# Kernel tuning notes

Measured on AMD Instinct MI355X. Metric: run time of the kernel, lower is better.

Reference implementation:

```python
import jax, jax.numpy as jnp
import numpy as np

N_NODES = 50000
D_IN = 128
HIDDEN = 128
UNITS_DENSE = 256
N_EDGES = 600000
N_PRED = 200000
N_SEL = 300000


def setup_inputs() -> dict:
    key = jax.random.key(0)
    ks = jax.random.split(key, 12)
    node_state = jax.random.normal(ks[0], (N_NODES, D_IN), jnp.float32)
    edge_index = jax.random.randint(ks[1], (2, N_EDGES), 0, N_NODES, jnp.int32)
    out_edges = jax.random.randint(ks[2], (2, N_PRED), 0, N_NODES, jnp.int32)
    set_idx = jnp.sort(jax.random.randint(ks[3], (N_SEL,), 0, 2 * N_PRED, jnp.int32))
    # Glorot-ish scaled weights
    W1 = jax.random.normal(ks[4], (D_IN, HIDDEN), jnp.float32) / np.float32(np.sqrt(D_IN))
    b1 = jnp.zeros((HIDDEN,), jnp.float32)
    W2 = jax.random.normal(ks[5], (HIDDEN, HIDDEN), jnp.float32) / np.float32(np.sqrt(HIDDEN))
    b2 = jnp.zeros((HIDDEN,), jnp.float32)
    dense_W = jax.random.normal(ks[6], (2 * 0 + HIDDEN, UNITS_DENSE), jnp.float32) / np.float32(np.sqrt(HIDDEN))
    dense_b = jnp.zeros((UNITS_DENSE,), jnp.float32)
    out_W = jax.random.normal(ks[7], (UNITS_DENSE, 2), jnp.float32) / np.float32(np.sqrt(UNITS_DENSE))
    out_b = jnp.zeros((2,), jnp.float32)
    return {
        "node_state": node_state, "edge_index": edge_index, "out_edges": out_edges,
        "set_idx": set_idx, "W1": W1, "b1": b1, "W2": W2, "b2": b2,
        "dense_W": dense_W, "dense_b": dense_b, "out_W": out_W, "out_b": out_b,
    }


def _graph_conv(h, src, dst, W, b):
    """DGL GraphConv, norm='both', no activation: D_in^{-1/2} A D_out^{-1/2} H W + b."""
    n = h.shape[0]
    ones = jnp.ones(src.shape[0], h.dtype)
    deg_out = jnp.clip(jax.ops.segment_sum(ones, src, num_segments=n), 1.0)  # [N]
    deg_in = jnp.clip(jax.ops.segment_sum(ones, dst, num_segments=n), 1.0)   # [N]
    h = (h * jax.lax.rsqrt(deg_out)[:, None]) @ W                            # [N, H]
    agg = jax.ops.segment_sum(h[src], dst, num_segments=n)                   # [N, H]
    return agg * jax.lax.rsqrt(deg_in)[:, None] + b


def reference(node_state, edge_index, out_edges, set_idx,
              W1, b1, W2, b2, dense_W, dense_b, out_W, out_b):
    src, dst = edge_index[0], edge_index[1]
    h = _graph_conv(node_state, src, dst, W1, b1)
    h = _graph_conv(h, src, dst, W2, b2)
    # concat along axis=0 as in the original: [2*E_pred, H]
    edge_state = jnp.concatenate([h[out_edges[0]], h[out_edges[1]]], axis=0)
    # boolean_mask replaced by equivalent gather of selected (True) rows
    edge_state_set = edge_state[set_idx]                                      # [N_SEL, H]
    hidden = jax.nn.relu(edge_state_set @ dense_W + dense_b)
    return jax.nn.softmax(hidden @ out_W + out_b, axis=-1)
```

## Files before the change

### kernel.cpp

```cpp
#include <hip/hip_runtime.h>

#define NN 50000
#define DD 128
#define NE 600000
#define NP 200000
#define NS 300000
#define NU 256
#define NBH 128
#define EPB 4688
#define NW 12500

typedef __attribute__((ext_vector_type(8))) short short8;
typedef __attribute__((ext_vector_type(4))) float floatx4;

__device__ inline float bf2f(unsigned int u16) {
    unsigned int x = u16 << 16;
    float f; __builtin_memcpy(&f, &x, 4); return f;
}
__device__ inline unsigned short f2bf(float f) {
    unsigned int x; __builtin_memcpy(&x, &f, 4);
    unsigned int lsb = (x >> 16) & 1u;
    x += 0x7fffu + lsb;
    return (unsigned short)(x >> 16);
}

__global__ __launch_bounds__(256) void k_hist(const int* __restrict__ ei,
                                              unsigned int* __restrict__ P) {
    __shared__ unsigned int hw[NW];
    int b = blockIdx.x, half = blockIdx.y, tid = threadIdx.x;
    for (int w = tid; w < NW; w += 256) hw[w] = 0;
    __syncthreads();
    const int* src = ei + (size_t)half * NE;
    int e0 = b * EPB, e1 = min(e0 + EPB, NE);
    for (int e = e0 + tid; e < e1; e += 256) {
        int s = src[e];
        atomicAdd(&hw[s >> 2], 1u << ((s & 3) * 8));
    }
    __syncthreads();
    unsigned int* Pb = P + ((size_t)half * NBH + b) * NW;
    for (int w = tid; w < NW; w += 256) Pb[w] = hw[w];
}

__global__ void k_reduce(const unsigned int* __restrict__ P, int* __restrict__ deg_in,
                         float* __restrict__ r) {
    int w = blockIdx.x * 256 + threadIdx.x;
    if (w >= 2 * NW) return;
    int half = (w >= NW);
    int wl = w - half * NW;
    const unsigned int* Ph = P + (size_t)half * NBH * NW + wl;
    int c0 = 0, c1 = 0, c2 = 0, c3 = 0;
    for (int b = 0; b < NBH; ++b) {
        unsigned int v = Ph[(size_t)b * NW];
        c0 += v & 0xff; c1 += (v >> 8) & 0xff; c2 += (v >> 16) & 0xff; c3 += v >> 24;
    }
    int nb = wl * 4;
    if (half) {
        int4 d = {c0, c1, c2, c3};
        *(int4*)(deg_in + nb) = d;
    }
    float4 rr = {rsqrtf((float)max(c0, 1)), rsqrtf((float)max(c1, 1)),
                 rsqrtf((float)max(c2, 1)), rsqrtf((float)max(c3, 1))};
    *(float4*)(r + (size_t)half * NN + nb) = rr;
}

__global__ __launch_bounds__(1024) void k_scan(const int* __restrict__ deg_in,
                                               int* __restrict__ row_ptr) {
    __shared__ int wsum[16];
    __shared__ int woff[16];
    __shared__ int carry_s;
    __shared__ int total_s;
    int tid = threadIdx.x, lane = tid & 63, w = tid >> 6;
    if (tid == 0) carry_s = 0;
    __syncthreads();
    for (int wb = 0; wb < NW; wb += 1024) {
        int i4 = wb + tid;
        int4 v = {0, 0, 0, 0};
        if (i4 < NW) v = *(const int4*)(deg_in + i4 * 4);
        int t0 = v.x, t1 = t0 + v.y, t2 = t1 + v.z, tot = t2 + v.w;
        int x = tot;
#pragma unroll
        for (int off = 1; off < 64; off <<= 1) {
            int y = __shfl_up(x, off);
            if (lane >= off) x += y;
        }
        if (lane == 63) wsum[w] = x;
        __syncthreads();
        if (w == 0 && lane < 16) {
            int s = wsum[lane];
            int xs = s;
#pragma unroll
            for (int off = 1; off < 16; off <<= 1) {
                int y = __shfl_up(xs, off);
                if (lane >= off) xs += y;
            }
            woff[lane] = xs - s;
            if (lane == 15) total_s = xs;
        }
        __syncthreads();
        if (i4 < NW) {
            int base = carry_s + woff[w] + x - tot;
            int4 o = {base, base + t0, base + t1, base + t2};
            *(int4*)(row_ptr + i4 * 4) = o;
        }
        __syncthreads();
        if (tid == 0) carry_s += total_s;
        __syncthreads();
    }
    if (tid == 0) row_ptr[NN] = carry_s;
}

__global__ void k_colscan(const unsigned int* __restrict__ Pin, const int* __restrict__ row_ptr,
                          int* __restrict__ basetab) {
    int n = blockIdx.x * 256 + threadIdx.x;
    if (n >= NN) return;
    int wl = n >> 2, sh = (n & 3) * 8;
    int run = row_ptr[n];
    for (int b = 0; b < NBH; ++b) {
        basetab[(size_t)b * NN + n] = run;
        run += (Pin[(size_t)b * NW + wl] >> sh) & 0xff;
    }
}

__global__ __launch_bounds__(256) void k_bucket2(const int* __restrict__ ei,
                                                 const int* __restrict__ basetab,
                                                 int* __restrict__ col) {
    __shared__ unsigned int cw[NW];
    int b = blockIdx.x, tid = threadIdx.x;
    for (int w = tid; w < NW; w += 256) cw[w] = 0;
    __syncthreads();
    const int* bt = basetab + (size_t)b * NN;
    int e0 = b * EPB, e1 = min(e0 + EPB, NE);
    for (int e = e0 + tid; e < e1; e += 256) {
        int s = ei[e], d = ei[NE + e];
        int sh = (d & 3) * 8;
        unsigned int old = atomicAdd(&cw[d >> 2], 1u << sh);
        int local = (old >> sh) & 0xff;
        col[bt[d] + local] = s;
    }
}

__global__ void k_castT(const float* __restrict__ src, unsigned short* __restrict__ dst,
                        int R, int C) {
    int t = blockIdx.x * 256 + threadIdx.x;
    if (t < R * C) {
        int r = t / C, c = t - r * C;
        dst[c * R + r] = f2bf(src[t]);
    }
}

template <bool ABF>
__global__ __launch_bounds__(256) void k_gemm_bf(const void* __restrict__ Ap,
                                                 const float* __restrict__ rs,
                                                 const unsigned short* __restrict__ BT,
                                                 unsigned short* __restrict__ Cm) {
    __shared__ unsigned short As[64][136];
    __shared__ unsigned short Bs[128][136];
    int tid = threadIdx.x, lane = tid & 63, wave = tid >> 6;
    int quad = lane >> 4, l16 = lane & 15;
    int row0 = blockIdx.x * 64;

    if (ABF) {
        const unsigned short* A = (const unsigned short*)Ap;
#pragma unroll
        for (int p = 0; p < 4; ++p) {
            int fid = tid + p * 256;
            int r = fid >> 4, c = fid & 15;
            int gr = row0 + r; if (gr > NN - 1) gr = NN - 1;
            *(uint4*)&As[r][c * 8] = *(const uint4*)(A + (size_t)gr * DD + c * 8);
        }
    } else {
        const float* A = (const float*)Ap;
#pragma unroll
        for (int p = 0; p < 8; ++p) {
            int fid = tid + p * 256;
            int r = fid >> 5, c = fid & 31;
            int gr = row0 + r; if (gr > NN - 1) gr = NN - 1;
            float4 v = *(const float4*)(A + (size_t)gr * DD + c * 4);
            ushort4 u;
            u.x = f2bf(v.x); u.y = f2bf(v.y); u.z = f2bf(v.z); u.w = f2bf(v.w);
            *(ushort4*)&As[r][c * 4] = u;
        }
    }
#pragma unroll
    for (int p = 0; p < 8; ++p) {
        int fid = tid + p * 256;
        int r = fid >> 4, c = fid & 15;
        *(uint4*)&Bs[r][c * 8] = *(const uint4*)(BT + (size_t)r * DD + c * 8);
    }
    __syncthreads();

    short8 af[4];
#pragma unroll
    for (int ks = 0; ks < 4; ++ks)
        af[ks] = *(const short8*)&As[wave * 16 + l16][ks * 32 + quad * 8];
    floatx4 acc[8];
#pragma unroll
    for (int nt = 0; nt < 8; ++nt) acc[nt] = (floatx4){0.f, 0.f, 0.f, 0.f};
#pragma unroll
    for (int ks = 0; ks < 4; ++ks) {
#pragma unroll
        for (int nt = 0; nt < 8; ++nt) {
            short8 bf = *(const short8*)&Bs[nt * 16 + l16][ks * 32 + quad * 8];
            acc[nt] = __builtin_amdgcn_mfma_f32_16x16x32_bf16(af[ks], bf, acc[nt], 0, 0, 0);
        }
    }
    int rbase = row0 + wave * 16 + quad * 4;
#pragma unroll
    for (int r = 0; r < 4; ++r) {
        int gr = rbase + r;
        if (gr < NN) {
            float s = rs[gr];
#pragma unroll
            for (int nt = 0; nt < 8; ++nt)
                Cm[(size_t)gr * DD + nt * 16 + l16] = f2bf(acc[nt][r] * s);
        }
    }
}

__global__ __launch_bounds__(256) void k_aggregate(const unsigned short* __restrict__ T,
                                                   const int* __restrict__ row_ptr,
                                                   const int* __restrict__ col,
                                                   const float* __restrict__ r_in,
                                                   const float* __restrict__ b,
                                                   unsigned short* __restrict__ H) {
    int node = blockIdx.x * 4 + (threadIdx.x >> 6);
    if (node >= NN) return;
    int lane = threadIdx.x & 63;
    int beg = row_ptr[node], end = row_ptr[node + 1];
    float a0 = 0.f, a1 = 0.f;
    for (int base = beg; base < end; base += 64) {
        int m = end - base; if (m > 64) m = 64;
        int myidx = (lane < m) ? col[base + lane] : 0;
        int j = 0;
        for (; j + 4 <= m; j += 4) {
            int s0 = __shfl(myidx, j), s1 = __shfl(myidx, j + 1);
            int s2 = __shfl(myidx, j + 2), s3 = __shfl(myidx, j + 3);
            unsigned int v0 = *(const unsigned int*)(T + (size_t)s0 * DD + lane * 2);
            unsigned int v1 = *(const unsigned int*)(T + (size_t)s1 * DD + lane * 2);
            unsigned int v2 = *(const unsigned int*)(T + (size_t)s2 * DD + lane * 2);
            unsigned int v3 = *(const unsigned int*)(T + (size_t)s3 * DD + lane * 2);
            a0 += bf2f(v0 & 0xffff) + bf2f(v1 & 0xffff) + bf2f(v2 & 0xffff) + bf2f(v3 & 0xffff);
            a1 += bf2f(v0 >> 16) + bf2f(v1 >> 16) + bf2f(v2 >> 16) + bf2f(v3 >> 16);
        }
        for (; j < m; ++j) {
            int s = __shfl(myidx, j);
            unsigned int v = *(const unsigned int*)(T + (size_t)s * DD + lane * 2);
            a0 += bf2f(v & 0xffff);
            a1 += bf2f(v >> 16);
        }
    }
    float rv = r_in[node];
    float o0 = a0 * rv + b[lane * 2];
    float o1 = a1 * rv + b[lane * 2 + 1];
    unsigned int packed = (unsigned int)f2bf(o0) | ((unsigned int)f2bf(o1) << 16);
    *(unsigned int*)(H + (size_t)node * DD + lane * 2) = packed;
}

__global__ __launch_bounds__(256) void k_mlp_mfma(const unsigned short* __restrict__ H2,
                                                  const unsigned short* __restrict__ BTd,
                                                  const float* __restrict__ db,
                                                  const float* __restrict__ oW,
                                                  const float* __restrict__ ob,
                                                  float* __restrict__ P) {
    __shared__ unsigned short As[64][136];
    __shared__ unsigned short Bs[128][136];
    int tid = threadIdx.x, lane = tid & 63, wave = tid >> 6;
    int quad = lane >> 4, l16 = lane & 15;
    int row0 = blockIdx.x * 64;
#pragma unroll
    for (int p = 0; p < 4; ++p) {
        int fid = tid + p * 256;
        int r = fid >> 4, c = fid & 15;
        int gr = row0 + r; if (gr > NN - 1) gr = NN - 1;
        *(uint4*)&As[r][c * 8] = *(const uint4*)(H2 + (size_t)gr * DD + c * 8);
    }
    short8 af[4];
    floatx4 acc[16];
#pragma unroll
    for (int i = 0; i < 16; ++i) acc[i] = (floatx4){0.f, 0.f, 0.f, 0.f};

    for (int ch = 0; ch < 2; ++ch) {
        __syncthreads();
#pragma unroll
        for (int p = 0; p < 8; ++p) {
            int fid = tid + p * 256;
            int r = fid >> 4, c = fid & 15;
            *(uint4*)&Bs[r][c * 8] = *(const uint4*)(BTd + (size_t)(ch * 128 + r) * DD + c * 8);
        }
        __syncthreads();
        if (ch == 0) {
#pragma unroll
            for (int ks = 0; ks < 4; ++ks)
                af[ks] = *(const short8*)&As[wave * 16 + l16][ks * 32 + quad * 8];
        }
#pragma unroll
        for (int ks = 0; ks < 4; ++ks) {
#pragma unroll
            for (int nt = 0; nt < 8; ++nt) {
                short8 bf = *(const short8*)&Bs[nt * 16 + l16][ks * 32 + quad * 8];
                acc[ch * 8 + nt] =
                    __builtin_amdgcn_mfma_f32_16x16x32_bf16(af[ks], bf, acc[ch * 8 + nt], 0, 0, 0);
            }
        }
    }
    int rbase = row0 + wave * 16 + quad * 4;
#pragma unroll
    for (int r = 0; r < 4; ++r) {
        float p0 = 0.f, p1 = 0.f;
#pragma unroll
        for (int ch = 0; ch < 2; ++ch) {
#pragma unroll
            for (int nt = 0; nt < 8; ++nt) {
                int colc = ch * 128 + nt * 16 + l16;
                float h = acc[ch * 8 + nt][r] + db[colc];
                h = fmaxf(h, 0.f);
                p0 += h * oW[2 * colc];
                p1 += h * oW[2 * colc + 1];
            }
        }
#pragma unroll
        for (int m = 8; m >= 1; m >>= 1) {
            p0 += __shfl_xor(p0, m, 16);
            p1 += __shfl_xor(p1, m, 16);
        }
        if (l16 == 0) {
            int gr = rbase + r;
            if (gr < NN) {
                float l0 = p0 + ob[0], l1 = p1 + ob[1];
                float mx = fmaxf(l0, l1);
                float e0 = __expf(l0 - mx), e1 = __expf(l1 - mx);
                float inv = 1.f / (e0 + e1);
                float2 pr = {e0 * inv, e1 * inv};
                *(float2*)(P + 2 * gr) = pr;
            }
        }
    }
}

__global__ void k_gather(const int* __restrict__ sidx, const int* __restrict__ oe,
                         const float* __restrict__ P, float* __restrict__ out) {
    int i = blockIdx.x * 256 + threadIdx.x;
    if (i >= NS) return;
    int node = oe[sidx[i]];
    float2 v = *(const float2*)(P + 2 * node);
    *(float2*)(out + 2 * i) = v;
}

extern "C" void kernel_launch(void* const* d_in, const int* in_sizes, int n_in,
                              void* d_out, int out_size, void* d_ws, size_t ws_size,
                              hipStream_t stream) {
    const float* node_state = (const float*)d_in[0];
    const int* ei   = (const int*)d_in[1];
    const int* oe   = (const int*)d_in[2];
    const int* sidx = (const int*)d_in[3];
    const float* W1 = (const float*)d_in[4];
    const float* b1 = (const float*)d_in[5];
    const float* W2 = (const float*)d_in[6];
    const float* b2 = (const float*)d_in[7];
    const float* dW = (const float*)d_in[8];
    const float* db = (const float*)d_in[9];
    const float* oW = (const float*)d_in[10];
    const float* ob = (const float*)d_in[11];
    float* out = (float*)d_out;

    char* ws = (char*)d_ws;
    size_t off = 0;
    auto carve = [&](size_t bytes) -> char* {
        char* p = ws + off;
        off = (off + bytes + 255) & ~(size_t)255;
        return p;
    };
    int*   deg_in  = (int*)carve((size_t)NN * 4);
    float* r       = (float*)carve((size_t)2 * NN * 4);
    int*   row_ptr = (int*)carve((size_t)(NN + 1) * 4);
    int*   col     = (int*)carve((size_t)NE * 4);
    unsigned int* P_hist = (unsigned int*)carve((size_t)2 * NBH * NW * 4);
    int*   basetab = (int*)carve((size_t)NBH * NN * 4);
    unsigned short* t   = (unsigned short*)carve((size_t)NN * DD * 2);
    unsigned short* h   = (unsigned short*)carve((size_t)NN * DD * 2);
    unsigned short* BT1 = (unsigned short*)carve((size_t)DD * DD * 2);
    unsigned short* BT2 = (unsigned short*)carve((size_t)DD * DD * 2);
    unsigned short* BTd = (unsigned short*)carve((size_t)DD * NU * 2);
    float* P = (float*)t;

    float* r_out = r;
    float* r_in  = r + NN;

    k_hist<<<dim3(NBH, 2), 256, 0, stream>>>(ei, P_hist);
    k_reduce<<<(2 * NW + 255) / 256, 256, 0, stream>>>(P_hist, deg_in, r);
    k_scan<<<1, 1024, 0, stream>>>(deg_in, row_ptr);
    k_colscan<<<(NN + 255) / 256, 256, 0, stream>>>(P_hist + (size_t)NBH * NW, row_ptr, basetab);
    k_bucket2<<<NBH, 256, 0, stream>>>(ei, basetab, col);

    k_castT<<<(DD * DD + 255) / 256, 256, 0, stream>>>(W1, BT1, DD, DD);
    k_castT<<<(DD * DD + 255) / 256, 256, 0, stream>>>(W2, BT2, DD, DD);
    k_castT<<<(DD * NU + 255) / 256, 256, 0, stream>>>(dW, BTd, DD, NU);

    k_gemm_bf<false><<<(NN + 63) / 64, 256, 0, stream>>>(node_state, r_out, BT1, t);
    k_aggregate<<<(NN + 3) / 4, 256, 0, stream>>>(t, row_ptr, col, r_in, b1, h);

    k_gemm_bf<true><<<(NN + 63) / 64, 256, 0, stream>>>(h, r_out, BT2, t);
    k_aggregate<<<(NN + 3) / 4, 256, 0, stream>>>(t, row_ptr, col, r_in, b2, h);

    k_mlp_mfma<<<(NN + 63) / 64, 256, 0, stream>>>(h, BTd, db, oW, ob, P);
    k_gather<<<(NS + 255) / 256, 256, 0, stream>>>(sidx, oe, P, out);
}
```

Measured before the change: 270.8 us.

## Vectorize aggregation with 16 lanes per node, merge weight casts, halve histogram blocks

The aggregation kernel now assigns 16 lanes per node, four nodes per wave, and each lane loads 16 bytes (8 bf16) per neighbor row. This replaces one node per wave with 4-byte loads, cutting memory instructions and shuffle overhead per gathered row. The three weight-cast launches are merged into one kernel, and the histogram/bucket block count drops from 128 to 64 with more edges per block. Fewer histogram blocks lowers the per-block partial-table traffic but gives less parallelism in the histogram and bucket phases.

```diff
diff --git a/kernel.cpp b/kernel.cpp
--- a/kernel.cpp
+++ b/kernel.cpp
@@ -6,9 +6,10 @@
 #define NP 200000
 #define NS 300000
 #define NU 256
-#define NBH 128
-#define EPB 4688
+#define NBH 64
+#define EPB 9375
 #define NW 12500
+#define NB64 782
 
 typedef __attribute__((ext_vector_type(8))) short short8;
 typedef __attribute__((ext_vector_type(4))) float floatx4;
@@ -139,12 +140,21 @@
     }
 }
 
-__global__ void k_castT(const float* __restrict__ src, unsigned short* __restrict__ dst,
-                        int R, int C) {
+__global__ void k_castW(const float* __restrict__ W1, const float* __restrict__ W2,
+                        const float* __restrict__ dW, unsigned short* __restrict__ BT1,
+                        unsigned short* __restrict__ BT2, unsigned short* __restrict__ BTd) {
     int t = blockIdx.x * 256 + threadIdx.x;
-    if (t < R * C) {
-        int r = t / C, c = t - r * C;
-        dst[c * R + r] = f2bf(src[t]);
+    if (t < 16384) {
+        int r = t >> 7, c = t & 127;
+        BT1[c * 128 + r] = f2bf(W1[t]);
+    } else if (t < 32768) {
+        int t2 = t - 16384;
+        int r = t2 >> 7, c = t2 & 127;
+        BT2[c * 128 + r] = f2bf(W2[t2]);
+    } else if (t < 65536) {
+        int t2 = t - 32768;
+        int r = t2 >> 8, c = t2 & 255;
+        BTd[c * 128 + r] = f2bf(dW[t2]);
     }
 }
 
@@ -223,37 +233,48 @@
                                                    const float* __restrict__ r_in,
                                                    const float* __restrict__ b,
                                                    unsigned short* __restrict__ H) {
-    int node = blockIdx.x * 4 + (threadIdx.x >> 6);
+    int wave = threadIdx.x >> 6, lane = threadIdx.x & 63;
+    int sub = lane >> 4, l16 = lane & 15;
+    int node = blockIdx.x * 16 + wave * 4 + sub;
     if (node >= NN) return;
-    int lane = threadIdx.x & 63;
     int beg = row_ptr[node], end = row_ptr[node + 1];
-    float a0 = 0.f, a1 = 0.f;
-    for (int base = beg; base < end; base += 64) {
-        int m = end - base; if (m > 64) m = 64;
-        int myidx = (lane < m) ? col[base + lane] : 0;
+    float a0 = 0.f, a1 = 0.f, a2 = 0.f, a3 = 0.f, a4 = 0.f, a5 = 0.f, a6 = 0.f, a7 = 0.f;
+    for (int base = beg; base < end; base += 16) {
+        int m = end - base; if (m > 16) m = 16;
+        int myidx = (l16 < m) ? col[base + l16] : 0;
         int j = 0;
-        for (; j + 4 <= m; j += 4) {
-            int s0 = __shfl(myidx, j), s1 = __shfl(myidx, j + 1);
-            int s2 = __shfl(myidx, j + 2), s3 = __shfl(myidx, j + 3);
-            unsigned int v0 = *(const unsigned int*)(T + (size_t)s0 * DD + lane * 2);
-            unsigned int v1 = *(const unsigned int*)(T + (size_t)s1 * DD + lane * 2);
-            unsigned int v2 = *(const unsigned int*)(T + (size_t)s2 * DD + lane * 2);
-            unsigned int v3 = *(const unsigned int*)(T + (size_t)s3 * DD + lane * 2);
-            a0 += bf2f(v0 & 0xffff) + bf2f(v1 & 0xffff) + bf2f(v2 & 0xffff) + bf2f(v3 & 0xffff);
-            a1 += bf2f(v0 >> 16) + bf2f(v1 >> 16) + bf2f(v2 >> 16) + bf2f(v3 >> 16);
-        }
-        for (; j < m; ++j) {
-            int s = __shfl(myidx, j);
-            unsigned int v = *(const unsigned int*)(T + (size_t)s * DD + lane * 2);
-            a0 += bf2f(v & 0xffff);
-            a1 += bf2f(v >> 16);
+        for (; j + 2 <= m; j += 2) {
+            int s0 = __shfl(myidx, (sub << 4) | j);
+            int s1 = __shfl(myidx, (sub << 4) | (j + 1));
+            uint4 v0 = *(const uint4*)(T + (size_t)s0 * DD + l16 * 8);
+            uint4 v1 = *(const uint4*)(T + (size_t)s1 * DD + l16 * 8);
+            a0 += bf2f(v0.x & 0xffff) + bf2f(v1.x & 0xffff);
+            a1 += bf2f(v0.x >> 16)    + bf2f(v1.x >> 16);
+            a2 += bf2f(v0.y & 0xffff) + bf2f(v1.y & 0xffff);
+            a3 += bf2f(v0.y >> 16)    + bf2f(v1.y >> 16);
+            a4 += bf2f(v0.z & 0xffff) + bf2f(v1.z & 0xffff);
+            a5 += bf2f(v0.z >> 16)    + bf2f(v1.z >> 16);
+            a6 += bf2f(v0.w & 0xffff) + bf2f(v1.w & 0xffff);
+            a7 += bf2f(v0.w >> 16)    + bf2f(v1.w >> 16);
+        }
+        if (j < m) {
+            int s0 = __shfl(myidx, (sub << 4) | j);
+            uint4 v0 = *(const uint4*)(T + (size_t)s0 * DD + l16 * 8);
+            a0 += bf2f(v0.x & 0xffff); a1 += bf2f(v0.x >> 16);
+            a2 += bf2f(v0.y & 0xffff); a3 += bf2f(v0.y >> 16);
+            a4 += bf2f(v0.z & 0xffff); a5 += bf2f(v0.z >> 16);
+            a6 += bf2f(v0.w & 0xffff); a7 += bf2f(v0.w >> 16);
         }
     }
     float rv = r_in[node];
-    float o0 = a0 * rv + b[lane * 2];
-    float o1 = a1 * rv + b[lane * 2 + 1];
-    unsigned int packed = (unsigned int)f2bf(o0) | ((unsigned int)f2bf(o1) << 16);
-    *(unsigned int*)(H + (size_t)node * DD + lane * 2) = packed;
+    float4 bl = *(const float4*)(b + l16 * 8);
+    float4 bh = *(const float4*)(b + l16 * 8 + 4);
+    uint4 w;
+    w.x = (unsigned int)f2bf(a0 * rv + bl.x) | ((unsigned int)f2bf(a1 * rv + bl.y) << 16);
+    w.y = (unsigned int)f2bf(a2 * rv + bl.z) | ((unsigned int)f2bf(a3 * rv + bl.w) << 16);
+    w.z = (unsigned int)f2bf(a4 * rv + bh.x) | ((unsigned int)f2bf(a5 * rv + bh.y) << 16);
+    w.w = (unsigned int)f2bf(a6 * rv + bh.z) | ((unsigned int)f2bf(a7 * rv + bh.w) << 16);
+    *(uint4*)(H + (size_t)node * DD + l16 * 8) = w;
 }
 
 __global__ __launch_bounds__(256) void k_mlp_mfma(const unsigned short* __restrict__ H2,
@@ -392,16 +413,14 @@
     k_colscan<<<(NN + 255) / 256, 256, 0, stream>>>(P_hist + (size_t)NBH * NW, row_ptr, basetab);
     k_bucket2<<<NBH, 256, 0, stream>>>(ei, basetab, col);
 
-    k_castT<<<(DD * DD + 255) / 256, 256, 0, stream>>>(W1, BT1, DD, DD);
-    k_castT<<<(DD * DD + 255) / 256, 256, 0, stream>>>(W2, BT2, DD, DD);
-    k_castT<<<(DD * NU + 255) / 256, 256, 0, stream>>>(dW, BTd, DD, NU);
-
-    k_gemm_bf<false><<<(NN + 63) / 64, 256, 0, stream>>>(node_state, r_out, BT1, t);
-    k_aggregate<<<(NN + 3) / 4, 256, 0, stream>>>(t, row_ptr, col, r_in, b1, h);
-
-    k_gemm_bf<true><<<(NN + 63) / 64, 256, 0, stream>>>(h, r_out, BT2, t);
-    k_aggregate<<<(NN + 3) / 4, 256, 0, stream>>>(t, row_ptr, col, r_in, b2, h);
-
-    k_mlp_mfma<<<(NN + 63) / 64, 256, 0, stream>>>(h, BTd, db, oW, ob, P);
+    k_castW<<<256, 256, 0, stream>>>(W1, W2, dW, BT1, BT2, BTd);
+
+    k_gemm_bf<false><<<NB64, 256, 0, stream>>>(node_state, r_out, BT1, t);
+    k_aggregate<<<(NN + 15) / 16, 256, 0, stream>>>(t, row_ptr, col, r_in, b1, h);
+
+    k_gemm_bf<true><<<NB64, 256, 0, stream>>>(h, r_out, BT2, t);
+    k_aggregate<<<(NN + 15) / 16, 256, 0, stream>>>(t, row_ptr, col, r_in, b2, h);
+
+    k_mlp_mfma<<<NB64, 256, 0, stream>>>(h, BTd, db, oW, ob, P);
     k_gather<<<(NS + 255) / 256, 256, 0, stream>>>(sidx, oe, P, out);
 }
```

Result: no change. 266.9 us (-1.4%).
